# Performance work log

Measured on AMD Instinct MI355X. Metric: run time of the kernel, lower is better.

## Reference

```python
import jax, jax.numpy as jnp
import numpy as np

HID = 256
NCLASS = 5
DEPTH = 11          # complete binary tree, N = 2**DEPTH - 1 nodes
BATCH = 128
N_NODES = 2 ** DEPTH - 1


def setup_inputs() -> dict:
    key = jax.random.key(0)
    ks = jax.random.split(key, 16)
    scale = 0.1
    def mat(k, shape):
        return scale * jax.random.normal(k, shape, dtype=jnp.float32)
    inp = {
        "x": jax.random.normal(ks[0], (BATCH, N_NODES, HID), dtype=jnp.float32),
        "W_i": mat(ks[1], (HID, HID)),
        "U_i": mat(ks[2], (2, HID, HID)),
        "b_i": jnp.zeros((HID,), jnp.float32),
        "W_f": mat(ks[3], (HID, HID)),
        "U_f": mat(ks[4], (2, 2, HID, HID)),
        "b_f": jnp.zeros((HID,), jnp.float32),
        "W_o": mat(ks[5], (HID, HID)),
        "U_o": mat(ks[6], (2, HID, HID)),
        "b_o": jnp.zeros((HID,), jnp.float32),
        "W_u": mat(ks[7], (HID, HID)),
        "U_u": mat(ks[8], (2, HID, HID)),
        "b_u": jnp.zeros((HID,), jnp.float32),
        "W_s": mat(ks[9], (NCLASS, HID)),
        "b_s": jnp.zeros((NCLASS,), jnp.float32),
    }
    return inp


def _mv(W, v):
    # W: [h,h] (or [c,h]), v: [B,M,h] -> [B,M,h_out]; matches U.mul(h).sum(dim=1)
    return jnp.einsum('ij,bmj->bmi', W, v)


def _tree_lstm(x, W_i, U_i, b_i, W_f, U_f, b_f, W_o, U_o, b_o, W_u, U_u, b_u):
    B, N, h = x.shape
    D = int(round(np.log2(N + 1)))
    h_all = jnp.zeros_like(x)   # init_tree: node_h = zeros
    c_all = jnp.zeros_like(x)   # init_tree: cell   = zeros
    for lvl in range(D - 1, -1, -1):  # bottom-up over tree levels
        s = 2 ** lvl - 1
        e = 2 ** (lvl + 1) - 1
        M = e - s
        x_lvl = x[:, s:e]                      # [B,M,h]
        if lvl == D - 1:  # leaves: children states are the zero-initialized ones
            hL = hR = cL = cR = jnp.zeros((B, M, h), x.dtype)
        else:
            # children of node i=s+j are at e+2j (left) and e+2j+1 (right)
            hc = h_all[:, e:e + 2 * M].reshape(B, M, 2, h)
            cc = c_all[:, e:e + 2 * M].reshape(B, M, 2, h)
            hL, hR = hc[:, :, 0], hc[:, :, 1]
            cL, cR = cc[:, :, 0], cc[:, :, 1]
        i_g = jax.nn.sigmoid(_mv(W_i, x_lvl) + _mv(U_i[0], hL) + _mv(U_i[1], hR) + b_i)
        o_g = jax.nn.sigmoid(_mv(W_o, x_lvl) + _mv(U_o[0], hL) + _mv(U_o[1], hR) + b_o)
        u_g = jnp.tanh(_mv(W_u, x_lvl) + _mv(U_u[0], hL) + _mv(U_u[1], hR) + b_u)
        Wfx = _mv(W_f, x_lvl)
        f0 = jax.nn.sigmoid(Wfx + _mv(U_f[0, 0], hL) + _mv(U_f[0, 1], hR) + b_f)
        f1 = jax.nn.sigmoid(Wfx + _mv(U_f[1, 0], hL) + _mv(U_f[1, 1], hR) + b_f)
        c_lvl = i_g * u_g + f0 * cL + f1 * cR
        h_lvl = o_g * jnp.tanh(c_lvl)
        h_all = h_all.at[:, s:e].set(h_lvl)
        c_all = c_all.at[:, s:e].set(c_lvl)
    return h_all


def reference(x, W_i, U_i, b_i, W_f, U_f, b_f, W_o, U_o, b_o, W_u, U_u, b_u, W_s, b_s):
    h_all = _tree_lstm(x, W_i, U_i, b_i, W_f, U_f, b_f, W_o, U_o, b_o, W_u, U_u, b_u)
    # PredictUpTree (dropout omitted for the deterministic reference):
    logits = jnp.einsum('ch,bnh->bnc', W_s, h_all) + b_s   # [B,N,Nclass]
    return jax.nn.softmax(logits, axis=-1)
```

## Files before the change

kernel.cpp:

```cpp
#include <hip/hip_runtime.h>
#include <math.h>

#define HID 256
#define NCLASS 5
#define DEPTH 11
#define NB 128
#define NN 2047

typedef __attribute__((ext_vector_type(8))) short bf16x8_t;
typedef __attribute__((ext_vector_type(4))) float f32x4_t;

__device__ __forceinline__ float bf2f(unsigned short u) {
    return __uint_as_float(((unsigned)u) << 16);
}
__device__ __forceinline__ unsigned short f2bf(float f) {
    unsigned x = __float_as_uint(f);
    unsigned r = (x + 0x7fff + ((x >> 16) & 1)) >> 16;
    return (unsigned short)r;
}
__device__ __forceinline__ float sigmoidf_(float x) {
    return 1.0f / (1.0f + __expf(-x));
}
__device__ __forceinline__ void gl_lds16(const void* g, void* l) {
    __builtin_amdgcn_global_load_lds(
        (const __attribute__((address_space(1))) unsigned int*)g,
        (__attribute__((address_space(3))) unsigned int*)l,
        16, 0, 0);
}

__global__ __launch_bounds__(256)
void prep_wcat(const float* __restrict__ W_i, const float* __restrict__ U_i,
               const float* __restrict__ W_f, const float* __restrict__ U_f,
               const float* __restrict__ W_o, const float* __restrict__ U_o,
               const float* __restrict__ W_u, const float* __restrict__ U_u,
               unsigned short* __restrict__ Wcat)
{
    int idx = blockIdx.x * 256 + threadIdx.x;
    int k = idx % 768;
    int n = idx / 768;
    int g = n >> 8;
    int ch = n & 255;
    int seg = k >> 8;
    int kk = k & 255;
    float v;
    if (seg == 0) {
        const float* W = (g == 0) ? W_i : (g == 1) ? W_o : (g == 2) ? W_u : W_f;
        v = W[ch * 256 + kk];
    } else {
        int side = seg - 1;
        if (g == 0)      v = U_i[(side * 256 + ch) * 256 + kk];
        else if (g == 1) v = U_o[(side * 256 + ch) * 256 + kk];
        else if (g == 2) v = U_u[(side * 256 + ch) * 256 + kk];
        else             v = U_f[(((g - 3) * 2 + side) * 256 + ch) * 256 + kk];
    }
    Wcat[(size_t)n * 768 + k] = f2bf(v);
}

__global__ __launch_bounds__(256)
void cast_x_kernel(const float* __restrict__ x, unsigned short* __restrict__ xb)
{
    size_t i = ((size_t)blockIdx.x * 256 + threadIdx.x) * 8;
    float4 a = *(const float4*)(x + i);
    float4 b = *(const float4*)(x + i + 4);
    unsigned short o[8] = {f2bf(a.x), f2bf(a.y), f2bf(a.z), f2bf(a.w),
                           f2bf(b.x), f2bf(b.y), f2bf(b.z), f2bf(b.w)};
    *(uint4*)(xb + i) = *(uint4*)o;
}

template<int NG, int NK, bool LEAF>
__global__ __launch_bounds__(512, 4)
void level_gemm(const unsigned short* __restrict__ xb,
                const unsigned short* __restrict__ hA,
                const unsigned short* __restrict__ Wcat,
                const float* __restrict__ c_child,
                const float* __restrict__ b_i, const float* __restrict__ b_o,
                const float* __restrict__ b_u, const float* __restrict__ b_f,
                float* __restrict__ c_out,
                unsigned short* __restrict__ hA_parent,
                unsigned short* __restrict__ h_all,
                int lgM)
{
    constexpr int NT = NG * 4;
    constexpr int BOFF = 8192;
    __shared__ __align__(16) char smem[BOFF + NT * 1024];

    const int tid  = threadIdx.x;
    const int w    = tid >> 6, lane = tid & 63;
    const int quad = lane >> 4, p = lane & 15;
    const int rh = w & 1, cq = w >> 1;
    const int chblk = blockIdx.x;
    const int R0 = blockIdx.y * 128;
    const int M = 1 << lgM, s = M - 1;

    const int arow = R0 + w * 16 + p;
    const int ab = arow >> lgM, am = arow & (M - 1);
    const unsigned short* a_x = xb + ((size_t)ab * NN + s + am) * 256 + quad * 8;
    const unsigned short* a_h = LEAF ? (const unsigned short*)nullptr
                                     : hA + (size_t)arow * 512 + quad * 8;
    const int nbt = LEAF ? (w < 4 ? 2 : 1) : (w < 4 ? 3 : 2);
    const int t0  = LEAF ? (w < 4 ? w * 2 : 8 + (w - 4))
                         : (w < 4 ? w * 3 : 12 + (w - 4) * 2);
    const unsigned short* bsrc[3];
    #pragma unroll
    for (int j = 0; j < 3; ++j) {
        int t = t0 + ((j < nbt) ? j : 0);
        int n = (t >> 2) * 256 + chblk * 64 + (t & 3) * 16 + p;
        bsrc[j] = Wcat + (size_t)n * 768 + quad * 8;
    }

    f32x4_t acc[4][NG];
    #pragma unroll
    for (int mi = 0; mi < 4; ++mi)
        #pragma unroll
        for (int j = 0; j < NG; ++j)
            acc[mi][j] = (f32x4_t){0.f, 0.f, 0.f, 0.f};

    for (int step = 0; step < NK; ++step) {
        const int k0 = step * 32;
        __syncthreads();
        const unsigned short* asrc = (LEAF || k0 < 256) ? (a_x + k0) : (a_h + (k0 - 256));
        gl_lds16(asrc, smem + w * 1024);
        #pragma unroll
        for (int j = 0; j < 3; ++j)
            if (j < nbt) gl_lds16(bsrc[j] + k0, smem + BOFF + (t0 + j) * 1024);
        __syncthreads();

        bf16x8_t af[4];
        #pragma unroll
        for (int mi = 0; mi < 4; ++mi)
            af[mi] = *(const bf16x8_t*)(smem + ((rh * 4 + mi) * 64 + lane) * 16);
        #pragma unroll
        for (int j = 0; j < NG; ++j) {
            bf16x8_t bfr = *(const bf16x8_t*)(smem + BOFF + ((j * 4 + cq) * 64 + lane) * 16);
            #pragma unroll
            for (int mi = 0; mi < 4; ++mi)
                acc[mi][j] = __builtin_amdgcn_mfma_f32_16x16x32_bf16(af[mi], bfr, acc[mi][j], 0, 0, 0);
        }
    }

    const int gch = chblk * 64 + cq * 16 + p;
    const float bi = b_i[gch], bo = b_o[gch], bu = b_u[gch];
    const float bfv = LEAF ? 0.f : b_f[gch];

    #pragma unroll
    for (int mi = 0; mi < 4; ++mi) {
        const int rowq = R0 + rh * 64 + mi * 16 + quad * 4;
        #pragma unroll
        for (int reg = 0; reg < 4; ++reg) {
            const int grow = rowq + reg;
            const int b = grow >> lgM, m = grow & (M - 1);
            float ig = sigmoidf_(acc[mi][0][reg] + bi);
            float og = sigmoidf_(acc[mi][1][reg] + bo);
            float ug = tanhf(acc[mi][2][reg] + bu);
            float c;
            if (LEAF) {
                c = ig * ug;
            } else {
                const float* crow = c_child + ((size_t)b * (M << 1) + 2 * m) * 256 + gch;
                float f0 = sigmoidf_(acc[mi][3][reg] + bfv);
                float f1 = sigmoidf_(acc[mi][4][reg] + bfv);
                c = fmaf(f0, crow[0], fmaf(f1, crow[256], ig * ug));
            }
            float h = og * tanhf(c);
            c_out[(size_t)grow * 256 + gch] = c;
            unsigned short hb = f2bf(h);
            h_all[((size_t)b * NN + s + m) * 256 + gch] = hb;
            if (hA_parent)
                hA_parent[((size_t)b * (M >> 1) + (m >> 1)) * 512 + (m & 1) * 256 + gch] = hb;
        }
    }
}

__global__ __launch_bounds__(256)
void softmax_kernel(const unsigned short* __restrict__ h_all,
                    const float* __restrict__ W_s, const float* __restrict__ b_s,
                    float* __restrict__ out)
{
    __shared__ float Ws[5 * 256];
    int tid = threadIdx.x;
    for (int i = tid; i < 1280; i += 256) Ws[i] = W_s[i];
    __syncthreads();

    int r = tid >> 3, q = tid & 7;
    size_t row = (size_t)blockIdx.x * 32 + r;
    const unsigned short* hp = h_all + row * 256 + q * 32;

    float p0 = 0.f, p1 = 0.f, p2 = 0.f, p3 = 0.f, p4 = 0.f;
    #pragma unroll
    for (int kk = 0; kk < 32; kk += 8) {
        uint4 raw = *(const uint4*)(hp + kk);
        unsigned short hu[8];
        *(uint4*)hu = raw;
        #pragma unroll
        for (int e = 0; e < 8; ++e) {
            float hvv = bf2f(hu[e]);
            int k = q * 32 + kk + e;
            p0 = fmaf(Ws[k],        hvv, p0);
            p1 = fmaf(Ws[256 + k],  hvv, p1);
            p2 = fmaf(Ws[512 + k],  hvv, p2);
            p3 = fmaf(Ws[768 + k],  hvv, p3);
            p4 = fmaf(Ws[1024 + k], hvv, p4);
        }
    }
    #pragma unroll
    for (int off = 4; off; off >>= 1) {
        p0 += __shfl_down(p0, off, 8);
        p1 += __shfl_down(p1, off, 8);
        p2 += __shfl_down(p2, off, 8);
        p3 += __shfl_down(p3, off, 8);
        p4 += __shfl_down(p4, off, 8);
    }
    if (q == 0) {
        float l0 = p0 + b_s[0], l1 = p1 + b_s[1], l2 = p2 + b_s[2];
        float l3 = p3 + b_s[3], l4 = p4 + b_s[4];
        float mx = fmaxf(fmaxf(fmaxf(l0, l1), fmaxf(l2, l3)), l4);
        float e0 = __expf(l0 - mx), e1 = __expf(l1 - mx), e2 = __expf(l2 - mx);
        float e3 = __expf(l3 - mx), e4 = __expf(l4 - mx);
        float inv = 1.0f / (e0 + e1 + e2 + e3 + e4);
        float* orow = out + row * NCLASS;
        orow[0] = e0 * inv;
        orow[1] = e1 * inv;
        orow[2] = e2 * inv;
        orow[3] = e3 * inv;
        orow[4] = e4 * inv;
    }
}

extern "C" void kernel_launch(void* const* d_in, const int* in_sizes, int n_in,
                              void* d_out, int out_size, void* d_ws, size_t ws_size,
                              hipStream_t stream) {
    const float* x   = (const float*)d_in[0];
    const float* W_i = (const float*)d_in[1];
    const float* U_i = (const float*)d_in[2];
    const float* b_i = (const float*)d_in[3];
    const float* W_f = (const float*)d_in[4];
    const float* U_f = (const float*)d_in[5];
    const float* b_f = (const float*)d_in[6];
    const float* W_o = (const float*)d_in[7];
    const float* U_o = (const float*)d_in[8];
    const float* b_o = (const float*)d_in[9];
    const float* W_u = (const float*)d_in[10];
    const float* U_u = (const float*)d_in[11];
    const float* b_u = (const float*)d_in[12];
    const float* W_s = (const float*)d_in[13];
    const float* b_s = (const float*)d_in[14];
    float* out = (float*)d_out;

    char* p = (char*)d_ws;
    unsigned short* Wcat  = (unsigned short*)p; p += 2097152;
    unsigned short* xb    = (unsigned short*)p; p += 134152192;
    unsigned short* h_all = (unsigned short*)p; p += 134152192;
    unsigned short* hA0   = (unsigned short*)p; p += 33554432;
    unsigned short* hA1   = (unsigned short*)p; p += 67108864;
    float* cb0 = (float*)p; p += 134217728;
    float* cb1 = (float*)p; p += 67108864;

    prep_wcat<<<3840, 256, 0, stream>>>(W_i, U_i, W_f, U_f, W_o, U_o, W_u, U_u, Wcat);
    cast_x_kernel<<<32752, 256, 0, stream>>>(x, xb);

    for (int lvl = DEPTH - 1; lvl >= 0; --lvl) {
        dim3 grid(4, 1 << lvl);
        float* c_o        = (lvl & 1) ? cb1 : cb0;
        const float* c_ch = ((lvl + 1) & 1) ? cb1 : cb0;
        const unsigned short* hA_this = (lvl & 1) ? hA1 : hA0;
        unsigned short* hA_par = (lvl > 0) ? (((lvl - 1) & 1) ? hA1 : hA0) : nullptr;

        if (lvl == DEPTH - 1) {
            level_gemm<3, 8, true><<<grid, 512, 0, stream>>>(
                xb, nullptr, Wcat, nullptr, b_i, b_o, b_u, b_f,
                c_o, hA_par, h_all, lvl);
        } else {
            level_gemm<5, 24, false><<<grid, 512, 0, stream>>>(
                xb, hA_this, Wcat, c_ch, b_i, b_o, b_u, b_f,
                c_o, hA_par, h_all, lvl);
        }
    }

    softmax_kernel<<<8188, 256, 0, stream>>>(h_all, W_s, b_s, out);
}
```

Measured before the change: 1.396 ms.

## Double-buffer LDS tiles in level GEMM and use fast sigmoid/tanh

Splits the level GEMM's shared-memory staging into two buffers, so the global-to-LDS load for step k+1 is issued before the MFMAs for step k. This drops one barrier per step and lets memory latency overlap compute. It also raises wave priority around the MFMA block and replaces tanhf and the sigmoid divide with fast exp/fdividef versions. The cost is twice the LDS per block, which may reduce occupancy, plus slightly lower accuracy in the activation functions.

```diff
diff --git a/kernel.cpp b/kernel.cpp
--- a/kernel.cpp
+++ b/kernel.cpp
@@ -19,7 +19,10 @@
     return (unsigned short)r;
 }
 __device__ __forceinline__ float sigmoidf_(float x) {
-    return 1.0f / (1.0f + __expf(-x));
+    return __fdividef(1.0f, 1.0f + __expf(-x));
+}
+__device__ __forceinline__ float tanhf_(float x) {
+    return 1.0f - __fdividef(2.0f, __expf(2.0f * x) + 1.0f);
 }
 __device__ __forceinline__ void gl_lds16(const void* g, void* l) {
     __builtin_amdgcn_global_load_lds(
@@ -82,7 +85,8 @@
 {
     constexpr int NT = NG * 4;
     constexpr int BOFF = 8192;
-    __shared__ __align__(16) char smem[BOFF + NT * 1024];
+    constexpr int BUFSZ = BOFF + NT * 1024;
+    __shared__ __align__(16) char smem[2 * BUFSZ];
 
     const int tid  = threadIdx.x;
     const int w    = tid >> 6, lane = tid & 63;
@@ -115,27 +119,41 @@
         for (int j = 0; j < NG; ++j)
             acc[mi][j] = (f32x4_t){0.f, 0.f, 0.f, 0.f};
 
+    {
+        gl_lds16(a_x, smem + w * 1024);
+        #pragma unroll
+        for (int j = 0; j < 3; ++j)
+            if (j < nbt) gl_lds16(bsrc[j], smem + BOFF + (t0 + j) * 1024);
+    }
+    __syncthreads();
+
     for (int step = 0; step < NK; ++step) {
-        const int k0 = step * 32;
-        __syncthreads();
-        const unsigned short* asrc = (LEAF || k0 < 256) ? (a_x + k0) : (a_h + (k0 - 256));
-        gl_lds16(asrc, smem + w * 1024);
-        #pragma unroll
-        for (int j = 0; j < 3; ++j)
-            if (j < nbt) gl_lds16(bsrc[j] + k0, smem + BOFF + (t0 + j) * 1024);
-        __syncthreads();
+        char* bufc = smem + (size_t)(step & 1) * BUFSZ;
+        if (step + 1 < NK) {
+            char* bufn = smem + (size_t)((step + 1) & 1) * BUFSZ;
+            const int k0 = (step + 1) * 32;
+            const unsigned short* asrc = (LEAF || k0 < 256) ? (a_x + k0) : (a_h + (k0 - 256));
+            gl_lds16(asrc, bufn + w * 1024);
+            #pragma unroll
+            for (int j = 0; j < 3; ++j)
+                if (j < nbt) gl_lds16(bsrc[j] + k0, bufn + BOFF + (t0 + j) * 1024);
+        }
+        __builtin_amdgcn_sched_barrier(0);
 
         bf16x8_t af[4];
         #pragma unroll
         for (int mi = 0; mi < 4; ++mi)
-            af[mi] = *(const bf16x8_t*)(smem + ((rh * 4 + mi) * 64 + lane) * 16);
+            af[mi] = *(const bf16x8_t*)(bufc + ((rh * 4 + mi) * 64 + lane) * 16);
+        __builtin_amdgcn_s_setprio(1);
         #pragma unroll
         for (int j = 0; j < NG; ++j) {
-            bf16x8_t bfr = *(const bf16x8_t*)(smem + BOFF + ((j * 4 + cq) * 64 + lane) * 16);
+            bf16x8_t bfr = *(const bf16x8_t*)(bufc + BOFF + ((j * 4 + cq) * 64 + lane) * 16);
             #pragma unroll
             for (int mi = 0; mi < 4; ++mi)
                 acc[mi][j] = __builtin_amdgcn_mfma_f32_16x16x32_bf16(af[mi], bfr, acc[mi][j], 0, 0, 0);
         }
+        __builtin_amdgcn_s_setprio(0);
+        __syncthreads();
     }
 
     const int gch = chblk * 64 + cq * 16 + p;
@@ -151,7 +169,7 @@
             const int b = grow >> lgM, m = grow & (M - 1);
             float ig = sigmoidf_(acc[mi][0][reg] + bi);
             float og = sigmoidf_(acc[mi][1][reg] + bo);
-            float ug = tanhf(acc[mi][2][reg] + bu);
+            float ug = tanhf_(acc[mi][2][reg] + bu);
             float c;
             if (LEAF) {
                 c = ig * ug;
@@ -161,7 +179,7 @@
                 float f1 = sigmoidf_(acc[mi][4][reg] + bfv);
                 c = fmaf(f0, crow[0], fmaf(f1, crow[256], ig * ug));
             }
-            float h = og * tanhf(c);
+            float h = og * tanhf_(c);
             c_out[(size_t)grow * 256 + gch] = c;
             unsigned short hb = f2bf(h);
             h_all[((size_t)b * NN + s + m) * 256 + gch] = hb;
```

Result: faster. 1.299 ms (-7.0%).
